# Optimization experiments

Measured on AMD Instinct MI355X. Metric: run time of the kernel, lower is better.

Reference implementation:

```python
import jax, jax.numpy as jnp
import numpy as np

EPS = 1e-12

def softmax_mask(x, mask, axis):
    # stable masked softmax: exp(x - max) * mask / (sum + eps)
    shift = jnp.max(x, axis=axis, keepdims=True)
    e = jnp.exp(x - shift) * mask
    return e / (jnp.sum(e, axis=axis, keepdims=True) + EPS)

def setup_inputs() -> dict:
    key = jax.random.key(0)
    kq, kk, kv, km = jax.random.split(key, 4)
    B, Lq, Lk, d, dv = 16, 2048, 2048, 128, 128
    q = jax.random.normal(kq, (B, Lq, d), dtype=jnp.float32)
    k = jax.random.normal(kk, (B, Lk, d), dtype=jnp.float32)
    v = jax.random.normal(kv, (B, Lk, dv), dtype=jnp.float32)
    mask = (jax.random.uniform(km, (B, Lq, Lk)) > 0.1).astype(jnp.float32)
    return {"q": q, "k": k, "v": v, "mask": mask}

def reference(q, k, v, mask):
    # attn[b,i,j] = q[b,i,:] . k[b,j,:]
    attn = jnp.einsum('bqd,bkd->bqk', q, k)
    col_attn = softmax_mask(attn, mask, axis=1)  # normalize over queries (columns)
    row_attn = softmax_mask(attn, mask, axis=2)  # normalize over keys (rows)
    gated = col_attn * row_attn
    output = jnp.einsum('bqk,bkd->bqd', gated, v)
    return (output, gated)
```

## Files before the change

kernel.cpp:

```cpp
#include <hip/hip_runtime.h>

#define BATCH 16
#define LSEQ  2048
#define DDIM  128
#define EPSV  1e-12f
#define NTILE (LSEQ / 64)
#define NROWS (BATCH * LSEQ)

typedef __attribute__((ext_vector_type(4))) float f32x4;
typedef __attribute__((ext_vector_type(8))) __bf16 bf16x8;
typedef __attribute__((ext_vector_type(8))) unsigned short u16x8;

__device__ __forceinline__ unsigned short f2bf(float x) {
    unsigned int u = __float_as_uint(x);
    u += 0x7FFFu + ((u >> 16) & 1u);
    return (unsigned short)(u >> 16);
}
__device__ __forceinline__ float bf2f(unsigned short h) {
    return __uint_as_float(((unsigned int)h) << 16);
}

__device__ __forceinline__ int swz(int row, int col8) {
    return (row << 6) + ((((col8 >> 3) ^ row) & 7) << 3);
}

__global__ __launch_bounds__(256) void k0_vtrans(
    const float* __restrict__ v,
    unsigned short* __restrict__ vth, unsigned short* __restrict__ vtl)
{
    const int b  = blockIdx.z;
    const int j0 = blockIdx.x * 64;
    const int d0 = blockIdx.y * 64;
    __shared__ float T[64][65];

    const int tid = threadIdx.x;
    {
        const int jr = tid >> 4;
        const int c4 = (tid & 15) << 2;
#pragma unroll
        for (int p = 0; p < 4; ++p) {
            const int row = jr + (p << 4);
            *(float4*)&T[row][c4] =
                *(const float4*)(v + ((size_t)b * LSEQ + j0 + row) * DDIM + d0 + c4);
        }
    }
    __syncthreads();

    const int dr = tid >> 2;
    const int jc = (tid & 3) << 4;
    u16x8 h[2], l[2];
#pragma unroll
    for (int e = 0; e < 16; ++e) {
        const float x = T[jc + e][dr];
        const unsigned short hh = f2bf(x);
        h[e >> 3][e & 7] = hh;
        l[e >> 3][e & 7] = f2bf(x - bf2f(hh));
    }
    unsigned short* oh = vth + ((size_t)b * DDIM + d0 + dr) * LSEQ + j0 + jc;
    unsigned short* ol = vtl + ((size_t)b * DDIM + d0 + dr) * LSEQ + j0 + jc;
    *(u16x8*)oh = h[0]; *(u16x8*)(oh + 8) = h[1];
    *(u16x8*)ol = l[0]; *(u16x8*)(ol + 8) = l[1];
}

__global__ __launch_bounds__(256, 2) void k1_qk_stats(
    const float* __restrict__ q, const float* __restrict__ kmat,
    const float* __restrict__ mask, float* __restrict__ attn,
    float* __restrict__ rowMt, float* __restrict__ rowSt,
    float* __restrict__ colMt, float* __restrict__ colSt)
{
    const int b  = blockIdx.z;
    const int it = blockIdx.y * 128;
    const int jt = blockIdx.x * 128;

    __shared__ __attribute__((aligned(16))) unsigned short smem[4 * 128 * 64];
    unsigned short* Ah = smem;
    unsigned short* Al = smem + 128 * 64;
    unsigned short* Bh = smem + 2 * 128 * 64;
    unsigned short* Bl = smem + 3 * 128 * 64;

    const int tid  = threadIdx.x;
    const int lane = tid & 63;
    const int w    = tid >> 6;
    const int wrow = (w >> 1) << 6;
    const int wcol = (w & 1) << 6;
    const int g    = lane >> 4;
    const int cl   = lane & 15;

    const float* qb = q    + ((size_t)b * LSEQ + it) * DDIM;
    const float* kb = kmat + ((size_t)b * LSEQ + jt) * DDIM;

    const int lr = tid >> 2;
    const int lc = (tid & 3) << 4;

    f32x4 acc[4][4];
    const f32x4 zero = {0.f, 0.f, 0.f, 0.f};
#pragma unroll
    for (int i = 0; i < 4; ++i)
#pragma unroll
        for (int j = 0; j < 4; ++j) acc[i][j] = zero;

    for (int ks2 = 0; ks2 < DDIM; ks2 += 64) {
        if (ks2) __syncthreads();
#pragma unroll
        for (int pr = 0; pr < 2; ++pr) {
            const int row = lr + (pr << 6);
            const float* qr = qb + (size_t)row * DDIM + ks2 + lc;
            const float* kr = kb + (size_t)row * DDIM + ks2 + lc;
#pragma unroll
            for (int cc = 0; cc < 16; cc += 8) {
                float xs[8], ys[8];
                *(float4*)&xs[0] = *(const float4*)(qr + cc);
                *(float4*)&xs[4] = *(const float4*)(qr + cc + 4);
                *(float4*)&ys[0] = *(const float4*)(kr + cc);
                *(float4*)&ys[4] = *(const float4*)(kr + cc + 4);
                u16x8 qh, ql, kh, kl;
#pragma unroll
                for (int e = 0; e < 8; ++e) {
                    const unsigned short h0 = f2bf(xs[e]);
                    qh[e] = h0;
                    ql[e] = f2bf(xs[e] - bf2f(h0));
                    const unsigned short h1 = f2bf(ys[e]);
                    kh[e] = h1;
                    kl[e] = f2bf(ys[e] - bf2f(h1));
                }
                const int o = swz(row, lc + cc);
                *(u16x8*)&Ah[o] = qh;
                *(u16x8*)&Al[o] = ql;
                *(u16x8*)&Bh[o] = kh;
                *(u16x8*)&Bl[o] = kl;
            }
        }
        __syncthreads();

#pragma unroll
        for (int ks = 0; ks < 64; ks += 32) {
            const int colb = ks + (g << 3);
            bf16x8 ah[4], al[4], bh[4], bl[4];
#pragma unroll
            for (int f = 0; f < 4; ++f) {
                const int ra = wrow + (f << 4) + cl;
                const int rb = wcol + (f << 4) + cl;
                ah[f] = __builtin_bit_cast(bf16x8, *(const u16x8*)&Ah[swz(ra, colb)]);
                al[f] = __builtin_bit_cast(bf16x8, *(const u16x8*)&Al[swz(ra, colb)]);
                bh[f] = __builtin_bit_cast(bf16x8, *(const u16x8*)&Bh[swz(rb, colb)]);
                bl[f] = __builtin_bit_cast(bf16x8, *(const u16x8*)&Bl[swz(rb, colb)]);
            }
#pragma unroll
            for (int fr = 0; fr < 4; ++fr)
#pragma unroll
                for (int fc = 0; fc < 4; ++fc) {
                    acc[fr][fc] = __builtin_amdgcn_mfma_f32_16x16x32_bf16(ah[fr], bh[fc], acc[fr][fc], 0, 0, 0);
                    acc[fr][fc] = __builtin_amdgcn_mfma_f32_16x16x32_bf16(ah[fr], bl[fc], acc[fr][fc], 0, 0, 0);
                    acc[fr][fc] = __builtin_amdgcn_mfma_f32_16x16x32_bf16(al[fr], bh[fc], acc[fr][fc], 0, 0, 0);
                }
        }
    }

    const size_t grow0 = (size_t)b * LSEQ + it + wrow;
    float*       arow  = attn + grow0 * LSEQ + jt + wcol;
    const float* mrow  = mask + grow0 * LSEQ + jt + wcol;

    float colm[4];
#pragma unroll
    for (int fc = 0; fc < 4; ++fc) {
        float m = acc[0][fc][0];
#pragma unroll
        for (int fr = 0; fr < 4; ++fr)
#pragma unroll
            for (int r = 0; r < 4; ++r) m = fmaxf(m, acc[fr][fc][r]);
        m = fmaxf(m, __shfl_xor(m, 16, 64));
        m = fmaxf(m, __shfl_xor(m, 32, 64));
        colm[fc] = m;
    }
    float rowm[4][4];
#pragma unroll
    for (int fr = 0; fr < 4; ++fr)
#pragma unroll
        for (int r = 0; r < 4; ++r) {
            float m = fmaxf(fmaxf(acc[fr][0][r], acc[fr][1][r]),
                            fmaxf(acc[fr][2][r], acc[fr][3][r]));
            m = fmaxf(m, __shfl_xor(m, 1, 64));
            m = fmaxf(m, __shfl_xor(m, 2, 64));
            m = fmaxf(m, __shfl_xor(m, 4, 64));
            m = fmaxf(m, __shfl_xor(m, 8, 64));
            rowm[fr][r] = m;
        }

    float cols_[4] = {0.f, 0.f, 0.f, 0.f};
    float rows_[4][4];
#pragma unroll
    for (int fr = 0; fr < 4; ++fr) {
#pragma unroll
        for (int r = 0; r < 4; ++r) {
            const int R = (fr << 4) + (g << 2) + r;
            float rs = 0.f;
#pragma unroll
            for (int fc = 0; fc < 4; ++fc) {
                const int C = (fc << 4) + cl;
                const float x = acc[fr][fc][r];
                arow[(size_t)R * LSEQ + C] = x;
                const float mk = mrow[(size_t)R * LSEQ + C];
                rs        += __expf(x - rowm[fr][r]) * mk;
                cols_[fc] += __expf(x - colm[fc])    * mk;
            }
            rs += __shfl_xor(rs, 1, 64);
            rs += __shfl_xor(rs, 2, 64);
            rs += __shfl_xor(rs, 4, 64);
            rs += __shfl_xor(rs, 8, 64);
            rows_[fr][r] = rs;
        }
    }
#pragma unroll
    for (int fc = 0; fc < 4; ++fc) {
        float s = cols_[fc];
        s += __shfl_xor(s, 16, 64);
        s += __shfl_xor(s, 32, 64);
        cols_[fc] = s;
    }

    const int ti = (blockIdx.y << 1) + (w >> 1);
    const int tj = (blockIdx.x << 1) + (w & 1);
    if (cl == 0) {
        const size_t rbase = (size_t)tj * NROWS + (size_t)b * LSEQ + it + wrow;
#pragma unroll
        for (int fr = 0; fr < 4; ++fr)
#pragma unroll
            for (int r = 0; r < 4; ++r) {
                const int R = (fr << 4) + (g << 2) + r;
                rowMt[rbase + R] = rowm[fr][r];
                rowSt[rbase + R] = rows_[fr][r];
            }
    }
    if (g == 0) {
        const size_t cbase = (size_t)ti * NROWS + (size_t)b * LSEQ + jt + wcol;
#pragma unroll
        for (int fc = 0; fc < 4; ++fc) {
            colMt[cbase + (fc << 4) + cl] = colm[fc];
            colSt[cbase + (fc << 4) + cl] = cols_[fc];
        }
    }
}

__global__ __launch_bounds__(256) void k2_combine(
    const float* __restrict__ rowMt, const float* __restrict__ rowSt,
    const float* __restrict__ colMt, const float* __restrict__ colSt,
    float* __restrict__ rmaxf, float* __restrict__ rsumf,
    float* __restrict__ cmaxf, float* __restrict__ csumf)
{
    const int id = blockIdx.x * 256 + threadIdx.x;
    const bool isRow = (id < NROWS);
    const int off = isRow ? id : id - NROWS;
    const float* Mt = isRow ? rowMt : colMt;
    const float* St = isRow ? rowSt : colSt;

    float m = -INFINITY;
#pragma unroll
    for (int t = 0; t < NTILE; ++t) m = fmaxf(m, Mt[(size_t)t * NROWS + off]);
    float s = 0.f;
#pragma unroll
    for (int t = 0; t < NTILE; ++t)
        s += St[(size_t)t * NROWS + off] * __expf(Mt[(size_t)t * NROWS + off] - m);

    if (isRow) { rmaxf[off] = m; rsumf[off] = s; }
    else       { cmaxf[off] = m; csumf[off] = s; }
}

__global__ __launch_bounds__(256, 2) void k3_gated_out(
    const float* __restrict__ mask,
    const unsigned short* __restrict__ vth, const unsigned short* __restrict__ vtl,
    const float* __restrict__ rmaxf, const float* __restrict__ cmaxf,
    const float* __restrict__ rsumf, const float* __restrict__ csumf,
    float* __restrict__ gated, float* __restrict__ outp)
{
    const int b   = blockIdx.y;
    const int it0 = blockIdx.x * 64;

    __shared__ __attribute__((aligned(16))) unsigned short Gh[64 * 64];
    __shared__ __attribute__((aligned(16))) unsigned short Gl[64 * 64];
    __shared__ __attribute__((aligned(16))) unsigned short Vh[128 * 64];
    __shared__ __attribute__((aligned(16))) unsigned short Vl[128 * 64];
    __shared__ float RowM[64], RowIS[64], ColM[64], ColIS[64];

    const int tid  = threadIdx.x;
    const int lane = tid & 63;
    const int w    = tid >> 6;
    const int g    = lane >> 4;
    const int cl   = lane & 15;

    if (tid < 64) {
        RowM[tid]  = rmaxf[b * LSEQ + it0 + tid];
        RowIS[tid] = 1.f / (rsumf[b * LSEQ + it0 + tid] + EPSV);
    }

    const int grow = tid >> 2;
    const int gcb  = (tid & 3) << 4;
    const int vrow = tid >> 1;
    const int vcb  = (tid & 1) << 5;

    float*       gb = gated + ((size_t)b * LSEQ + it0) * LSEQ;
    const float* mb = mask  + ((size_t)b * LSEQ + it0) * LSEQ;
    const unsigned short* vhb = vth + ((size_t)b * DDIM + vrow) * LSEQ;
    const unsigned short* vlb = vtl + ((size_t)b * DDIM + vrow) * LSEQ;

    f32x4 acc[4][2];
    const f32x4 zero = {0.f, 0.f, 0.f, 0.f};
#pragma unroll
    for (int i = 0; i < 4; ++i) { acc[i][0] = zero; acc[i][1] = zero; }

    float4 xr[4], mr[4];
#pragma unroll
    for (int p = 0; p < 4; ++p) {
        xr[p] = *(const float4*)(gb + (size_t)grow * LSEQ + gcb + p * 4);
        mr[p] = *(const float4*)(mb + (size_t)grow * LSEQ + gcb + p * 4);
    }

#pragma unroll 1
    for (int j0 = 0; j0 < LSEQ; j0 += 64) {
        __syncthreads();
        if (tid < 64) {
            ColM[tid]  = cmaxf[b * LSEQ + j0 + tid];
            ColIS[tid] = 1.f / (csumf[b * LSEQ + j0 + tid] + EPSV);
        }
#pragma unroll
        for (int cc = 0; cc < 32; cc += 8) {
            *(u16x8*)&Vh[swz(vrow, vcb + cc)] = *(const u16x8*)(vhb + j0 + vcb + cc);
            *(u16x8*)&Vl[swz(vrow, vcb + cc)] = *(const u16x8*)(vlb + j0 + vcb + cc);
        }
        __syncthreads();

        const float mrw = RowM[grow], isr = RowIS[grow];
        float gs[16];
#pragma unroll
        for (int p = 0; p < 4; ++p) {
            const float xs[4] = {xr[p].x, xr[p].y, xr[p].z, xr[p].w};
            const float ms[4] = {mr[p].x, mr[p].y, mr[p].z, mr[p].w};
#pragma unroll
            for (int e = 0; e < 4; ++e) {
                const int c = gcb + p * 4 + e;
                gs[p * 4 + e] = ms[e] * __expf(2.f * xs[e] - mrw - ColM[c]) * isr * ColIS[c];
            }
            *(float4*)(gb + (size_t)grow * LSEQ + j0 + gcb + p * 4) =
                make_float4(gs[p * 4], gs[p * 4 + 1], gs[p * 4 + 2], gs[p * 4 + 3]);
        }
#pragma unroll
        for (int cc = 0; cc < 16; cc += 8) {
            u16x8 hh, ll;
#pragma unroll
            for (int e = 0; e < 8; ++e) {
                const unsigned short hb = f2bf(gs[cc + e]);
                hh[e] = hb;
                ll[e] = f2bf(gs[cc + e] - bf2f(hb));
            }
            *(u16x8*)&Gh[swz(grow, gcb + cc)] = hh;
            *(u16x8*)&Gl[swz(grow, gcb + cc)] = ll;
        }
        if (j0 + 64 < LSEQ) {
#pragma unroll
            for (int p = 0; p < 4; ++p) {
                xr[p] = *(const float4*)(gb + (size_t)grow * LSEQ + j0 + 64 + gcb + p * 4);
                mr[p] = *(const float4*)(mb + (size_t)grow * LSEQ + j0 + 64 + gcb + p * 4);
            }
        }
        __syncthreads();

#pragma unroll
        for (int ks = 0; ks < 64; ks += 32) {
            const int colb = ks + (g << 3);
            bf16x8 ah[4], al[4], bh[2], bl[2];
#pragma unroll
            for (int f = 0; f < 4; ++f) {
                const int ra = (f << 4) + cl;
                ah[f] = __builtin_bit_cast(bf16x8, *(const u16x8*)&Gh[swz(ra, colb)]);
                al[f] = __builtin_bit_cast(bf16x8, *(const u16x8*)&Gl[swz(ra, colb)]);
            }
#pragma unroll
            for (int f = 0; f < 2; ++f) {
                const int rb = (w << 5) + (f << 4) + cl;
                bh[f] = __builtin_bit_cast(bf16x8, *(const u16x8*)&Vh[swz(rb, colb)]);
                bl[f] = __builtin_bit_cast(bf16x8, *(const u16x8*)&Vl[swz(rb, colb)]);
            }
#pragma unroll
            for (int fr = 0; fr < 4; ++fr)
#pragma unroll
                for (int fc = 0; fc < 2; ++fc) {
                    acc[fr][fc] = __builtin_amdgcn_mfma_f32_16x16x32_bf16(ah[fr], bh[fc], acc[fr][fc], 0, 0, 0);
                    acc[fr][fc] = __builtin_amdgcn_mfma_f32_16x16x32_bf16(al[fr], bh[fc], acc[fr][fc], 0, 0, 0);
                    acc[fr][fc] = __builtin_amdgcn_mfma_f32_16x16x32_bf16(ah[fr], bl[fc], acc[fr][fc], 0, 0, 0);
                }
        }
    }

    float* ob = outp + ((size_t)b * LSEQ + it0) * DDIM + (w << 5);
#pragma unroll
    for (int fr = 0; fr < 4; ++fr)
#pragma unroll
        for (int r = 0; r < 4; ++r) {
            const int R = (fr << 4) + (g << 2) + r;
#pragma unroll
            for (int fc = 0; fc < 2; ++fc)
                ob[(size_t)R * DDIM + (fc << 4) + cl] = acc[fr][fc][r];
        }
}

extern "C" void kernel_launch(void* const* d_in, const int* in_sizes, int n_in,
                              void* d_out, int out_size, void* d_ws, size_t ws_size,
                              hipStream_t stream)
{
    (void)in_sizes; (void)n_in; (void)out_size; (void)ws_size;
    const float* q    = (const float*)d_in[0];
    const float* k    = (const float*)d_in[1];
    const float* v    = (const float*)d_in[2];
    const float* mask = (const float*)d_in[3];

    float* outp  = (float*)d_out;
    float* gated = (float*)d_out + (size_t)BATCH * LSEQ * DDIM;

    float* rowMt = (float*)d_ws;
    float* rowSt = rowMt + (size_t)NTILE * NROWS;
    float* colMt = rowSt + (size_t)NTILE * NROWS;
    float* colSt = colMt + (size_t)NTILE * NROWS;
    float* rmaxf = colSt + (size_t)NTILE * NROWS;
    float* rsumf = rmaxf + NROWS;
    float* cmaxf = rsumf + NROWS;
    float* csumf = cmaxf + NROWS;
    unsigned short* vth = (unsigned short*)(csumf + NROWS);
    unsigned short* vtl = vth + (size_t)BATCH * DDIM * LSEQ;

    dim3 g0(LSEQ / 64, DDIM / 64, BATCH);
    k0_vtrans<<<g0, dim3(256), 0, stream>>>(v, vth, vtl);

    dim3 g1(LSEQ / 128, LSEQ / 128, BATCH);
    k1_qk_stats<<<g1, dim3(256), 0, stream>>>(q, k, mask, gated,
                                              rowMt, rowSt, colMt, colSt);

    k2_combine<<<dim3(2 * NROWS / 256), dim3(256), 0, stream>>>(
        rowMt, rowSt, colMt, colSt, rmaxf, rsumf, cmaxf, csumf);

    dim3 g3(LSEQ / 64, BATCH);
    k3_gated_out<<<g3, dim3(256), 0, stream>>>(mask, vth, vtl, rmaxf, cmaxf,
                                               rsumf, csumf, gated, outp);
}
```

Before: 751.3 us.

## Pre-split Q/K to bf16 planes, fold mask into attn, stream via LDS-direct loads

Adds a kernel that splits Q and K into bf16 hi/lo planes once, so the QK kernel loads them with global_load_lds straight into swizzled LDS instead of converting each tile in registers. The mask is prefetched into registers and folded into the stored attention by writing a large negative value for masked entries. The gated-output kernel then no longer reads the mask, uses precomputed inverse sums, takes 32-row tiles with occupancy 3, and loads V tiles via LDS-direct. The cost is extra workspace and a pre-pass over Q/K. It relies on exp of -1e30 underflowing to zero to reproduce the masking.

```diff
diff --git a/kernel.cpp b/kernel.cpp
--- a/kernel.cpp
+++ b/kernel.cpp
@@ -6,6 +6,7 @@
 #define EPSV  1e-12f
 #define NTILE (LSEQ / 64)
 #define NROWS (BATCH * LSEQ)
+#define MASKED_NEG (-1e30f)
 
 typedef __attribute__((ext_vector_type(4))) float f32x4;
 typedef __attribute__((ext_vector_type(8))) __bf16 bf16x8;
@@ -22,6 +23,35 @@
 
 __device__ __forceinline__ int swz(int row, int col8) {
     return (row << 6) + ((((col8 >> 3) ^ row) & 7) << 3);
+}
+
+__device__ __forceinline__ void gll16(const unsigned short* src, unsigned short* ldsdst) {
+    __builtin_amdgcn_global_load_lds(
+        (const __attribute__((address_space(1))) void*)src,
+        (__attribute__((address_space(3))) void*)ldsdst, 16, 0, 0);
+}
+
+__global__ __launch_bounds__(256) void k0_split(
+    const float* __restrict__ q, const float* __restrict__ kmat,
+    unsigned short* __restrict__ qh, unsigned short* __restrict__ ql,
+    unsigned short* __restrict__ kh, unsigned short* __restrict__ kl)
+{
+    const float* s     = blockIdx.y ? kmat : q;
+    unsigned short* ph = blockIdx.y ? kh : qh;
+    unsigned short* pl = blockIdx.y ? kl : ql;
+    const size_t i = ((size_t)blockIdx.x * 256 + threadIdx.x) << 3;
+    float xs[8];
+    *(float4*)&xs[0] = *(const float4*)(s + i);
+    *(float4*)&xs[4] = *(const float4*)(s + i + 4);
+    u16x8 hh, ll;
+#pragma unroll
+    for (int e = 0; e < 8; ++e) {
+        const unsigned short h = f2bf(xs[e]);
+        hh[e] = h;
+        ll[e] = f2bf(xs[e] - bf2f(h));
+    }
+    *(u16x8*)(ph + i) = hh;
+    *(u16x8*)(pl + i) = ll;
 }
 
 __global__ __launch_bounds__(256) void k0_vtrans(
@@ -63,7 +93,8 @@
 }
 
 __global__ __launch_bounds__(256, 2) void k1_qk_stats(
-    const float* __restrict__ q, const float* __restrict__ kmat,
+    const unsigned short* __restrict__ qh, const unsigned short* __restrict__ ql,
+    const unsigned short* __restrict__ kh, const unsigned short* __restrict__ kl,
     const float* __restrict__ mask, float* __restrict__ attn,
     float* __restrict__ rowMt, float* __restrict__ rowSt,
     float* __restrict__ colMt, float* __restrict__ colSt)
@@ -74,9 +105,9 @@
 
     __shared__ __attribute__((aligned(16))) unsigned short smem[4 * 128 * 64];
     unsigned short* Ah = smem;
-    unsigned short* Al = smem + 128 * 64;
-    unsigned short* Bh = smem + 2 * 128 * 64;
-    unsigned short* Bl = smem + 3 * 128 * 64;
+    unsigned short* Al = smem + 8192;
+    unsigned short* Bh = smem + 16384;
+    unsigned short* Bl = smem + 24576;
 
     const int tid  = threadIdx.x;
     const int lane = tid & 63;
@@ -86,11 +117,11 @@
     const int g    = lane >> 4;
     const int cl   = lane & 15;
 
-    const float* qb = q    + ((size_t)b * LSEQ + it) * DDIM;
-    const float* kb = kmat + ((size_t)b * LSEQ + jt) * DDIM;
-
-    const int lr = tid >> 2;
-    const int lc = (tid & 3) << 4;
+    const unsigned short* splane = (w == 0) ? qh : (w == 1) ? ql : (w == 2) ? kh : kl;
+    const size_t srow0 = (size_t)b * LSEQ + ((w < 2) ? it : jt);
+    unsigned short* dplane = smem + w * 8192;
+    const int srow = lane >> 3;
+    const int sslt = lane & 7;
 
     f32x4 acc[4][4];
     const f32x4 zero = {0.f, 0.f, 0.f, 0.f};
@@ -99,36 +130,29 @@
 #pragma unroll
         for (int j = 0; j < 4; ++j) acc[i][j] = zero;
 
-    for (int ks2 = 0; ks2 < DDIM; ks2 += 64) {
-        if (ks2) __syncthreads();
-#pragma unroll
-        for (int pr = 0; pr < 2; ++pr) {
-            const int row = lr + (pr << 6);
-            const float* qr = qb + (size_t)row * DDIM + ks2 + lc;
-            const float* kr = kb + (size_t)row * DDIM + ks2 + lc;
-#pragma unroll
-            for (int cc = 0; cc < 16; cc += 8) {
-                float xs[8], ys[8];
-                *(float4*)&xs[0] = *(const float4*)(qr + cc);
-                *(float4*)&xs[4] = *(const float4*)(qr + cc + 4);
-                *(float4*)&ys[0] = *(const float4*)(kr + cc);
-                *(float4*)&ys[4] = *(const float4*)(kr + cc + 4);
-                u16x8 qh, ql, kh, kl;
-#pragma unroll
-                for (int e = 0; e < 8; ++e) {
-                    const unsigned short h0 = f2bf(xs[e]);
-                    qh[e] = h0;
-                    ql[e] = f2bf(xs[e] - bf2f(h0));
-                    const unsigned short h1 = f2bf(ys[e]);
-                    kh[e] = h1;
-                    kl[e] = f2bf(ys[e] - bf2f(h1));
-                }
-                const int o = swz(row, lc + cc);
-                *(u16x8*)&Ah[o] = qh;
-                *(u16x8*)&Al[o] = ql;
-                *(u16x8*)&Bh[o] = kh;
-                *(u16x8*)&Bl[o] = kl;
-            }
+    float mreg[4][4][4];
+    const float* mrow = mask + ((size_t)b * LSEQ + it + wrow) * LSEQ + jt + wcol;
+
+#pragma unroll
+    for (int half = 0; half < 2; ++half) {
+        const int ks2 = half << 6;
+        if (half) __syncthreads();
+#pragma unroll
+        for (int qq = 0; qq < 16; ++qq) {
+            const int row = (qq << 3) + srow;
+            const int ss  = sslt ^ (row & 7);
+            gll16(splane + (srow0 + row) * DDIM + ks2 + (ss << 3),
+                  dplane + (qq << 9));
+        }
+        if (half) {
+#pragma unroll
+            for (int fr = 0; fr < 4; ++fr)
+#pragma unroll
+                for (int r = 0; r < 4; ++r)
+#pragma unroll
+                    for (int fc = 0; fc < 4; ++fc)
+                        mreg[fr][r][fc] =
+                            mrow[(size_t)((fr << 4) + (g << 2) + r) * LSEQ + (fc << 4) + cl];
         }
         __syncthreads();
 
@@ -156,9 +180,7 @@
         }
     }
 
-    const size_t grow0 = (size_t)b * LSEQ + it + wrow;
-    float*       arow  = attn + grow0 * LSEQ + jt + wcol;
-    const float* mrow  = mask + grow0 * LSEQ + jt + wcol;
+    float* arow = attn + ((size_t)b * LSEQ + it + wrow) * LSEQ + jt + wcol;
 
     float colm[4];
 #pragma unroll
@@ -193,15 +215,16 @@
 #pragma unroll
         for (int r = 0; r < 4; ++r) {
             const int R = (fr << 4) + (g << 2) + r;
+            const float rm = rowm[fr][r];
             float rs = 0.f;
 #pragma unroll
             for (int fc = 0; fc < 4; ++fc) {
                 const int C = (fc << 4) + cl;
-                const float x = acc[fr][fc][r];
-                arow[(size_t)R * LSEQ + C] = x;
-                const float mk = mrow[(size_t)R * LSEQ + C];
-                rs        += __expf(x - rowm[fr][r]) * mk;
-                cols_[fc] += __expf(x - colm[fc])    * mk;
+                const float x  = acc[fr][fc][r];
+                const float xp = (mreg[fr][r][fc] != 0.f) ? x : MASKED_NEG;
+                arow[(size_t)R * LSEQ + C] = xp;
+                rs        += __expf(xp - rm);
+                cols_[fc] += __expf(xp - colm[fc]);
             }
             rs += __shfl_xor(rs, 1, 64);
             rs += __shfl_xor(rs, 2, 64);
@@ -244,8 +267,8 @@
 __global__ __launch_bounds__(256) void k2_combine(
     const float* __restrict__ rowMt, const float* __restrict__ rowSt,
     const float* __restrict__ colMt, const float* __restrict__ colSt,
-    float* __restrict__ rmaxf, float* __restrict__ rsumf,
-    float* __restrict__ cmaxf, float* __restrict__ csumf)
+    float* __restrict__ rmaxf, float* __restrict__ rinvf,
+    float* __restrict__ cmaxf, float* __restrict__ cinvf)
 {
     const int id = blockIdx.x * 256 + threadIdx.x;
     const bool isRow = (id < NROWS);
@@ -260,26 +283,25 @@
 #pragma unroll
     for (int t = 0; t < NTILE; ++t)
         s += St[(size_t)t * NROWS + off] * __expf(Mt[(size_t)t * NROWS + off] - m);
-
-    if (isRow) { rmaxf[off] = m; rsumf[off] = s; }
-    else       { cmaxf[off] = m; csumf[off] = s; }
-}
-
-__global__ __launch_bounds__(256, 2) void k3_gated_out(
-    const float* __restrict__ mask,
+    const float inv = 1.f / (s + EPSV);
+
+    if (isRow) { rmaxf[off] = m; rinvf[off] = inv; }
+    else       { cmaxf[off] = m; cinvf[off] = inv; }
+}
+
+__global__ __launch_bounds__(256, 3) void k3_gated_out(
     const unsigned short* __restrict__ vth, const unsigned short* __restrict__ vtl,
     const float* __restrict__ rmaxf, const float* __restrict__ cmaxf,
-    const float* __restrict__ rsumf, const float* __restrict__ csumf,
+    const float* __restrict__ rinvf, const float* __restrict__ cinvf,
     float* __restrict__ gated, float* __restrict__ outp)
 {
     const int b   = blockIdx.y;
-    const int it0 = blockIdx.x * 64;
-
-    __shared__ __attribute__((aligned(16))) unsigned short Gh[64 * 64];
-    __shared__ __attribute__((aligned(16))) unsigned short Gl[64 * 64];
+    const int it0 = blockIdx.x * 32;
+
+    __shared__ __attribute__((aligned(16))) unsigned short Gh[32 * 64];
+    __shared__ __attribute__((aligned(16))) unsigned short Gl[32 * 64];
     __shared__ __attribute__((aligned(16))) unsigned short Vh[128 * 64];
     __shared__ __attribute__((aligned(16))) unsigned short Vl[128 * 64];
-    __shared__ float RowM[64], RowIS[64], ColM[64], ColIS[64];
 
     const int tid  = threadIdx.x;
     const int lane = tid & 63;
@@ -287,100 +309,95 @@
     const int g    = lane >> 4;
     const int cl   = lane & 15;
 
-    if (tid < 64) {
-        RowM[tid]  = rmaxf[b * LSEQ + it0 + tid];
-        RowIS[tid] = 1.f / (rsumf[b * LSEQ + it0 + tid] + EPSV);
-    }
-
-    const int grow = tid >> 2;
-    const int gcb  = (tid & 3) << 4;
-    const int vrow = tid >> 1;
-    const int vcb  = (tid & 1) << 5;
-
-    float*       gb = gated + ((size_t)b * LSEQ + it0) * LSEQ;
-    const float* mb = mask  + ((size_t)b * LSEQ + it0) * LSEQ;
-    const unsigned short* vhb = vth + ((size_t)b * DDIM + vrow) * LSEQ;
-    const unsigned short* vlb = vtl + ((size_t)b * DDIM + vrow) * LSEQ;
-
-    f32x4 acc[4][2];
+    const int grow = tid >> 3;
+    const int gcb  = (tid & 7) << 3;
+
+    const float mrw = rmaxf[b * LSEQ + it0 + grow];
+    const float irw = rinvf[b * LSEQ + it0 + grow];
+
+    float* gb = gated + ((size_t)b * LSEQ + it0) * LSEQ;
+
+    unsigned short* vplane_d       = (w >> 1) ? Vl : Vh;
+    const unsigned short* vplane_s = (w >> 1) ? vtl : vth;
+    const int vrow0 = (w & 1) << 6;
+    const int srow  = lane >> 3;
+    const int sslt  = lane & 7;
+
+    f32x4 acc[2][2];
     const f32x4 zero = {0.f, 0.f, 0.f, 0.f};
 #pragma unroll
-    for (int i = 0; i < 4; ++i) { acc[i][0] = zero; acc[i][1] = zero; }
-
-    float4 xr[4], mr[4];
-#pragma unroll
-    for (int p = 0; p < 4; ++p) {
-        xr[p] = *(const float4*)(gb + (size_t)grow * LSEQ + gcb + p * 4);
-        mr[p] = *(const float4*)(mb + (size_t)grow * LSEQ + gcb + p * 4);
+    for (int i = 0; i < 2; ++i) { acc[i][0] = zero; acc[i][1] = zero; }
+
+    float4 xn[2], cmn[2], cin[2];
+#pragma unroll
+    for (int p = 0; p < 2; ++p) {
+        xn[p]  = *(const float4*)(gb + (size_t)grow * LSEQ + gcb + (p << 2));
+        cmn[p] = *(const float4*)(cmaxf + b * LSEQ + gcb + (p << 2));
+        cin[p] = *(const float4*)(cinvf + b * LSEQ + gcb + (p << 2));
     }
 
 #pragma unroll 1
     for (int j0 = 0; j0 < LSEQ; j0 += 64) {
         __syncthreads();
-        if (tid < 64) {
-            ColM[tid]  = cmaxf[b * LSEQ + j0 + tid];
-            ColIS[tid] = 1.f / (csumf[b * LSEQ + j0 + tid] + EPSV);
-        }
-#pragma unroll
-        for (int cc = 0; cc < 32; cc += 8) {
-            *(u16x8*)&Vh[swz(vrow, vcb + cc)] = *(const u16x8*)(vhb + j0 + vcb + cc);
-            *(u16x8*)&Vl[swz(vrow, vcb + cc)] = *(const u16x8*)(vlb + j0 + vcb + cc);
-        }
-        __syncthreads();
-
-        const float mrw = RowM[grow], isr = RowIS[grow];
-        float gs[16];
-#pragma unroll
-        for (int p = 0; p < 4; ++p) {
-            const float xs[4] = {xr[p].x, xr[p].y, xr[p].z, xr[p].w};
-            const float ms[4] = {mr[p].x, mr[p].y, mr[p].z, mr[p].w};
-#pragma unroll
-            for (int e = 0; e < 4; ++e) {
-                const int c = gcb + p * 4 + e;
-                gs[p * 4 + e] = ms[e] * __expf(2.f * xs[e] - mrw - ColM[c]) * isr * ColIS[c];
+#pragma unroll
+        for (int qq = 0; qq < 8; ++qq) {
+            const int row = vrow0 + (qq << 3) + srow;
+            const int ss  = sslt ^ (row & 7);
+            gll16(vplane_s + ((size_t)b * DDIM + row) * LSEQ + j0 + (ss << 3),
+                  vplane_d + (((vrow0 >> 3) + qq) << 9));
+        }
+
+        float4 xc[2], cmc[2], cic[2];
+#pragma unroll
+        for (int p = 0; p < 2; ++p) { xc[p] = xn[p]; cmc[p] = cmn[p]; cic[p] = cin[p]; }
+        if (j0 + 64 < LSEQ) {
+#pragma unroll
+            for (int p = 0; p < 2; ++p) {
+                xn[p]  = *(const float4*)(gb + (size_t)grow * LSEQ + j0 + 64 + gcb + (p << 2));
+                cmn[p] = *(const float4*)(cmaxf + b * LSEQ + j0 + 64 + gcb + (p << 2));
+                cin[p] = *(const float4*)(cinvf + b * LSEQ + j0 + 64 + gcb + (p << 2));
             }
-            *(float4*)(gb + (size_t)grow * LSEQ + j0 + gcb + p * 4) =
-                make_float4(gs[p * 4], gs[p * 4 + 1], gs[p * 4 + 2], gs[p * 4 + 3]);
-        }
-#pragma unroll
-        for (int cc = 0; cc < 16; cc += 8) {
-            u16x8 hh, ll;
-#pragma unroll
-            for (int e = 0; e < 8; ++e) {
-                const unsigned short hb = f2bf(gs[cc + e]);
-                hh[e] = hb;
-                ll[e] = f2bf(gs[cc + e] - bf2f(hb));
-            }
-            *(u16x8*)&Gh[swz(grow, gcb + cc)] = hh;
-            *(u16x8*)&Gl[swz(grow, gcb + cc)] = ll;
-        }
-        if (j0 + 64 < LSEQ) {
-#pragma unroll
-            for (int p = 0; p < 4; ++p) {
-                xr[p] = *(const float4*)(gb + (size_t)grow * LSEQ + j0 + 64 + gcb + p * 4);
-                mr[p] = *(const float4*)(mb + (size_t)grow * LSEQ + j0 + 64 + gcb + p * 4);
-            }
-        }
+        }
+
+        float gs[8];
+#pragma unroll
+        for (int p = 0; p < 2; ++p) {
+            const float xs[4]  = {xc[p].x, xc[p].y, xc[p].z, xc[p].w};
+            const float cms[4] = {cmc[p].x, cmc[p].y, cmc[p].z, cmc[p].w};
+            const float cis[4] = {cic[p].x, cic[p].y, cic[p].z, cic[p].w};
+#pragma unroll
+            for (int e = 0; e < 4; ++e)
+                gs[(p << 2) + e] = __expf(2.f * xs[e] - mrw - cms[e]) * irw * cis[e];
+            *(float4*)(gb + (size_t)grow * LSEQ + j0 + gcb + (p << 2)) =
+                make_float4(gs[(p << 2)], gs[(p << 2) + 1], gs[(p << 2) + 2], gs[(p << 2) + 3]);
+        }
+        u16x8 hh, ll;
+#pragma unroll
+        for (int e = 0; e < 8; ++e) {
+            const unsigned short hb = f2bf(gs[e]);
+            hh[e] = hb;
+            ll[e] = f2bf(gs[e] - bf2f(hb));
+        }
+        *(u16x8*)&Gh[swz(grow, gcb)] = hh;
+        *(u16x8*)&Gl[swz(grow, gcb)] = ll;
+
         __syncthreads();
 
 #pragma unroll
         for (int ks = 0; ks < 64; ks += 32) {
             const int colb = ks + (g << 3);
-            bf16x8 ah[4], al[4], bh[2], bl[2];
-#pragma unroll
-            for (int f = 0; f < 4; ++f) {
+            bf16x8 ah[2], al[2], bh[2], bl[2];
+#pragma unroll
+            for (int f = 0; f < 2; ++f) {
                 const int ra = (f << 4) + cl;
                 ah[f] = __builtin_bit_cast(bf16x8, *(const u16x8*)&Gh[swz(ra, colb)]);
                 al[f] = __builtin_bit_cast(bf16x8, *(const u16x8*)&Gl[swz(ra, colb)]);
-            }
-#pragma unroll
-            for (int f = 0; f < 2; ++f) {
                 const int rb = (w << 5) + (f << 4) + cl;
                 bh[f] = __builtin_bit_cast(bf16x8, *(const u16x8*)&Vh[swz(rb, colb)]);
                 bl[f] = __builtin_bit_cast(bf16x8, *(const u16x8*)&Vl[swz(rb, colb)]);
             }
 #pragma unroll
-            for (int fr = 0; fr < 4; ++fr)
+            for (int fr = 0; fr < 2; ++fr)
 #pragma unroll
                 for (int fc = 0; fc < 2; ++fc) {
                     acc[fr][fc] = __builtin_amdgcn_mfma_f32_16x16x32_bf16(ah[fr], bh[fc], acc[fr][fc], 0, 0, 0);
@@ -392,7 +409,7 @@
 
     float* ob = outp + ((size_t)b * LSEQ + it0) * DDIM + (w << 5);
 #pragma unroll
-    for (int fr = 0; fr < 4; ++fr)
+    for (int fr = 0; fr < 2; ++fr)
 #pragma unroll
         for (int r = 0; r < 4; ++r) {
             const int R = (fr << 4) + (g << 2) + r;
@@ -420,23 +437,30 @@
     float* colMt = rowSt + (size_t)NTILE * NROWS;
     float* colSt = colMt + (size_t)NTILE * NROWS;
     float* rmaxf = colSt + (size_t)NTILE * NROWS;
-    float* rsumf = rmaxf + NROWS;
-    float* cmaxf = rsumf + NROWS;
-    float* csumf = cmaxf + NROWS;
-    unsigned short* vth = (unsigned short*)(csumf + NROWS);
+    float* rinvf = rmaxf + NROWS;
+    float* cmaxf = rinvf + NROWS;
+    float* cinvf = cmaxf + NROWS;
+    unsigned short* vth = (unsigned short*)(cinvf + NROWS);
     unsigned short* vtl = vth + (size_t)BATCH * DDIM * LSEQ;
+    unsigned short* qhp = vtl + (size_t)BATCH * DDIM * LSEQ;
+    unsigned short* qlp = qhp + (size_t)BATCH * LSEQ * DDIM;
+    unsigned short* khp = qlp + (size_t)BATCH * LSEQ * DDIM;
+    unsigned short* klp = khp + (size_t)BATCH * LSEQ * DDIM;
+
+    dim3 gsplit((BATCH * LSEQ * DDIM) / 2048, 2);
+    k0_split<<<gsplit, dim3(256), 0, stream>>>(q, k, qhp, qlp, khp, klp);
 
     dim3 g0(LSEQ / 64, DDIM / 64, BATCH);
     k0_vtrans<<<g0, dim3(256), 0, stream>>>(v, vth, vtl);
 
     dim3 g1(LSEQ / 128, LSEQ / 128, BATCH);
-    k1_qk_stats<<<g1, dim3(256), 0, stream>>>(q, k, mask, gated,
+    k1_qk_stats<<<g1, dim3(256), 0, stream>>>(qhp, qlp, khp, klp, mask, gated,
                                               rowMt, rowSt, colMt, colSt);
 
     k2_combine<<<dim3(2 * NROWS / 256), dim3(256), 0, stream>>>(
-        rowMt, rowSt, colMt, colSt, rmaxf, rsumf, cmaxf, csumf);
-
-    dim3 g3(LSEQ / 64, BATCH);
-    k3_gated_out<<<g3, dim3(256), 0, stream>>>(mask, vth, vtl, rmaxf, cmaxf,
-                                               rsumf, csumf, gated, outp);
-}
+        rowMt, rowSt, colMt, colSt, rmaxf, rinvf, cmaxf, cinvf);
+
+    dim3 g3(LSEQ / 32, BATCH);
+    k3_gated_out<<<g3, dim3(256), 0, stream>>>(vth, vtl, rmaxf, cmaxf,
+                                               rinvf, cinvf, gated, outp);
+}
```

Measured after the change: 693.5 us. 7.7% less time.
